# Optimization experiments

Hardware: AMD Instinct MI355X
Metric: run time of the kernel (lower is better)

Reference implementation:

```python
import jax, jax.numpy as jnp
import numpy as np

B, L, HID = 2, 2048, 2048
NH, NKV, HD = 16, 4, 128
LAT = 512
Q_PER_KV = NH // NKV
SCALE = HD ** -0.5
ROPE_THETA = 10000.0


def setup_inputs() -> dict:
    key = jax.random.key(0)
    ks = jax.random.split(key, 6)
    s = lambda fan_in: 1.0 / np.sqrt(fan_in)
    return {
        "x": jax.random.normal(ks[0], (B, L, HID), dtype=jnp.float32),
        "Wq": jax.random.normal(ks[1], (HID, NH * HD), dtype=jnp.float32) * s(HID),
        "Wc": jax.random.normal(ks[2], (HID, LAT), dtype=jnp.float32) * s(HID),
        "Wk": jax.random.normal(ks[3], (LAT, NKV * HD), dtype=jnp.float32) * s(LAT),
        "Wv": jax.random.normal(ks[4], (LAT, NKV * HD), dtype=jnp.float32) * s(LAT),
        "Wo": jax.random.normal(ks[5], (NH * HD, HID), dtype=jnp.float32) * s(NH * HD),
        "attention_mask": jnp.ones((B, L), dtype=jnp.int32),
    }


def _rope(t):  # t: [B, H, L, HD]
    half = HD // 2
    inv_freq = 1.0 / (ROPE_THETA ** (jnp.arange(half, dtype=jnp.float32) / half))
    pos = jnp.arange(t.shape[2], dtype=jnp.float32)
    freqs = pos[:, None] * inv_freq[None, :]          # [L, half]
    cos = jnp.cos(freqs)[None, None].astype(t.dtype)  # [1,1,L,half]
    sin = jnp.sin(freqs)[None, None].astype(t.dtype)
    t1, t2 = t[..., :half], t[..., half:]
    return jnp.concatenate([t1 * cos - t2 * sin, t2 * cos + t1 * sin], axis=-1)


def reference(x, Wq, Wc, Wk, Wv, Wo, attention_mask):
    q = (x @ Wq).reshape(B, L, NH, HD).transpose(0, 2, 1, 3)      # [B,NH,L,HD]
    c = x @ Wc                                                    # latent bottleneck
    k = (c @ Wk).reshape(B, L, NKV, HD).transpose(0, 2, 1, 3)     # [B,NKV,L,HD]
    v = (c @ Wv).reshape(B, L, NKV, HD).transpose(0, 2, 1, 3)
    # GQA repeat_interleave along head axis
    k = jnp.repeat(k, Q_PER_KV, axis=1)                           # [B,NH,L,HD]
    v = jnp.repeat(v, Q_PER_KV, axis=1)
    q = _rope(q)
    k = _rope(k)
    att = jnp.einsum("bhqd,bhkd->bhqk", q, k) * SCALE             # [B,NH,L,L]
    neg = jnp.finfo(att.dtype).min
    causal = jnp.tril(jnp.ones((L, L), dtype=bool))[None, None]
    att = jnp.where(causal, att, neg)
    key_mask = (attention_mask > 0)[:, None, None, :]             # [B,1,1,L]
    att = jnp.where(key_mask, att, neg)
    att = jax.nn.softmax(att, axis=-1)
    y = jnp.einsum("bhqk,bhkd->bhqd", att, v)
    y = y.transpose(0, 2, 1, 3).reshape(B, L, NH * HD)
    return y @ Wo
```

## Files before the change

kernel.cpp:

```cpp
#include <hip/hip_runtime.h>
#include <hip/hip_bf16.h>
#include <cstdint>
#include <cstddef>

#define B_    2
#define L_    2048
#define HID_  2048
#define NH_   16
#define NKV_  4
#define HD_   128
#define LAT_  512
#define SCALE_ 0.08838834764831845f
#define SC2_   0.1275174365f

typedef unsigned short u16;
typedef unsigned int   u32;
typedef __attribute__((ext_vector_type(8))) short   short8;
typedef __attribute__((ext_vector_type(4))) float   floatx4;

typedef __attribute__((address_space(1))) const u32 gas_u32;
typedef __attribute__((address_space(3))) u32       las_u32;

__device__ __forceinline__ void gl_lds16(const u16* g, u16* l) {
    __builtin_amdgcn_global_load_lds((gas_u32*)g, (las_u32*)l, 16, 0, 0);
}

__device__ __forceinline__ float bf2f(u16 u) {
    union { u32 i; float f; } v; v.i = ((u32)u) << 16; return v.f;
}
__device__ __forceinline__ u16 f2bf(float f) {
    union { float f; u32 u; } v; v.f = f;
    u32 u = v.u;
    u32 r = (u + 0x7fffu + ((u >> 16) & 1u)) >> 16;
    return (u16)r;
}

__global__ void cvt_kernel(const float* __restrict__ in, u16* __restrict__ out, int n) {
    int i = blockIdx.x * 256 + threadIdx.x;
    if (i < n) out[i] = f2bf(in[i]);
}

__global__ void cvt_transpose_kernel(const float* __restrict__ in, u16* __restrict__ out,
                                     int R, int C) {
    __shared__ u16 tile[32][33];
    int c0 = blockIdx.x * 32, r0 = blockIdx.y * 32;
    int tx = threadIdx.x & 31, ty = threadIdx.x >> 5;
    for (int i = ty; i < 32; i += 8)
        tile[tx][i] = f2bf(in[(size_t)(r0 + i) * C + c0 + tx]);
    __syncthreads();
    for (int i = ty; i < 32; i += 8)
        out[(size_t)(c0 + i) * R + r0 + tx] = tile[i][tx];
}

__global__ void transpose_v_kernel(const u16* __restrict__ in, u16* __restrict__ out) {
    __shared__ u16 t[32][33];
    int lt = blockIdx.x, dt = blockIdx.y, bh = blockIdx.z;
    int b = bh >> 2, kvh = bh & 3;
    int tx = threadIdx.x & 31, ty = threadIdx.x >> 5;
    for (int i = ty; i < 32; i += 8)
        t[i][tx] = in[(((size_t)b * L_ + lt * 32 + i) * NKV_ + kvh) * HD_ + dt * 32 + tx];
    __syncthreads();
    for (int i = ty; i < 32; i += 8)
        out[((size_t)bh * HD_ + dt * 32 + i) * L_ + lt * 32 + tx] = t[tx][i];
}

template<int OUT_BF16>
__global__ __launch_bounds__(256)
void gemm_bt(const u16* __restrict__ A, const u16* __restrict__ BT,
             void* __restrict__ C, int M, int N, int K) {
    __shared__ __align__(16) u16 As[128][32];
    __shared__ __align__(16) u16 Bs[128][32];
    const int tid  = threadIdx.x;
    const int m0   = blockIdx.y * 128, n0 = blockIdx.x * 128;
    const int wave = tid >> 6, lane = tid & 63;
    const int wm   = (wave >> 1) * 64, wn = (wave & 1) * 64;
    const int quad = lane >> 4, l16 = lane & 15;

    const int srow = wave * 32 + (lane >> 2);
    const int scol = (lane & 3) * 8;
    const u16* aptr0 = A  + (size_t)(m0 + srow) * K + scol;
    const u16* bptr0 = BT + (size_t)(n0 + srow) * K + scol;
    const u16* aptr1 = aptr0 + (size_t)16 * K;
    const u16* bptr1 = bptr0 + (size_t)16 * K;
    u16* lA0 = &As[wave * 32][0];
    u16* lA1 = &As[wave * 32 + 16][0];
    u16* lB0 = &Bs[wave * 32][0];
    u16* lB1 = &Bs[wave * 32 + 16][0];

    floatx4 acc[4][4] = {};

    for (int k0 = 0; k0 < K; k0 += 32) {
        gl_lds16(aptr0 + k0, lA0);
        gl_lds16(aptr1 + k0, lA1);
        gl_lds16(bptr0 + k0, lB0);
        gl_lds16(bptr1 + k0, lB1);
        __syncthreads();

        short8 af[4], bfr[4];
        #pragma unroll
        for (int i = 0; i < 4; i++) af[i]  = *(const short8*)&As[wm + i * 16 + l16][quad * 8];
        #pragma unroll
        for (int i = 0; i < 4; i++) bfr[i] = *(const short8*)&Bs[wn + i * 16 + l16][quad * 8];
        #pragma unroll
        for (int mi = 0; mi < 4; mi++)
            #pragma unroll
            for (int ni = 0; ni < 4; ni++)
                acc[mi][ni] = __builtin_amdgcn_mfma_f32_16x16x32_bf16(
                    af[mi], bfr[ni], acc[mi][ni], 0, 0, 0);
        __syncthreads();
    }

    #pragma unroll
    for (int mi = 0; mi < 4; mi++) {
        #pragma unroll
        for (int ni = 0; ni < 4; ni++) {
            #pragma unroll
            for (int r = 0; r < 4; r++) {
                int row = m0 + wm + mi * 16 + quad * 4 + r;
                int col = n0 + wn + ni * 16 + l16;
                float v = acc[mi][ni][r];
                if (OUT_BF16) ((u16*)C)[(size_t)row * N + col] = f2bf(v);
                else          ((float*)C)[(size_t)row * N + col] = v;
            }
        }
    }
}

__global__ __launch_bounds__(256)
void gemm_bt_split(const u16* __restrict__ A, const u16* __restrict__ BT,
                   u16* __restrict__ C0, u16* __restrict__ C1,
                   int M, int N, int K, int Nsplit, int N0, int N1) {
    __shared__ __align__(16) u16 As[128][32];
    __shared__ __align__(16) u16 Bs[128][32];
    const int tid  = threadIdx.x;
    const int m0   = blockIdx.y * 128, n0 = blockIdx.x * 128;
    const int wave = tid >> 6, lane = tid & 63;
    const int wm   = (wave >> 1) * 64, wn = (wave & 1) * 64;
    const int quad = lane >> 4, l16 = lane & 15;

    const int srow = wave * 32 + (lane >> 2);
    const int scol = (lane & 3) * 8;
    const u16* aptr0 = A  + (size_t)(m0 + srow) * K + scol;
    const u16* bptr0 = BT + (size_t)(n0 + srow) * K + scol;
    const u16* aptr1 = aptr0 + (size_t)16 * K;
    const u16* bptr1 = bptr0 + (size_t)16 * K;
    u16* lA0 = &As[wave * 32][0];
    u16* lA1 = &As[wave * 32 + 16][0];
    u16* lB0 = &Bs[wave * 32][0];
    u16* lB1 = &Bs[wave * 32 + 16][0];

    floatx4 acc[4][4] = {};

    for (int k0 = 0; k0 < K; k0 += 32) {
        gl_lds16(aptr0 + k0, lA0);
        gl_lds16(aptr1 + k0, lA1);
        gl_lds16(bptr0 + k0, lB0);
        gl_lds16(bptr1 + k0, lB1);
        __syncthreads();

        short8 af[4], bfr[4];
        #pragma unroll
        for (int i = 0; i < 4; i++) af[i]  = *(const short8*)&As[wm + i * 16 + l16][quad * 8];
        #pragma unroll
        for (int i = 0; i < 4; i++) bfr[i] = *(const short8*)&Bs[wn + i * 16 + l16][quad * 8];
        #pragma unroll
        for (int mi = 0; mi < 4; mi++)
            #pragma unroll
            for (int ni = 0; ni < 4; ni++)
                acc[mi][ni] = __builtin_amdgcn_mfma_f32_16x16x32_bf16(
                    af[mi], bfr[ni], acc[mi][ni], 0, 0, 0);
        __syncthreads();
    }

    const int side = (n0 >= Nsplit);
    u16* Cw = side ? C1 : C0;
    const int nw = side ? N1 : N0;
    const int cbase = side ? Nsplit : 0;

    #pragma unroll
    for (int mi = 0; mi < 4; mi++) {
        #pragma unroll
        for (int ni = 0; ni < 4; ni++) {
            #pragma unroll
            for (int r = 0; r < 4; r++) {
                int row = m0 + wm + mi * 16 + quad * 4 + r;
                int col = n0 + wn + ni * 16 + l16 - cbase;
                Cw[(size_t)row * nw + col] = f2bf(acc[mi][ni][r]);
            }
        }
    }
}

__global__ void rope_perm(const u16* __restrict__ in, u16* __restrict__ out,
                          int nh, int nhbits) {
    int idx = blockIdx.x * 256 + threadIdx.x;
    int d = idx & 63;
    int l = (idx >> 6) & (L_ - 1);
    int h = (idx >> 17) & (nh - 1);
    int b = idx >> (17 + nhbits);
    const u16* src = &in[(((size_t)b * L_ + l) * nh + h) * HD_];
    u16* dst = &out[(((size_t)b * nh + h) * L_ + l) * HD_];
    float t1 = bf2f(src[d]), t2 = bf2f(src[d + 64]);
    float inv = expf(-(float)d * 0.14391156831212787f);
    float fr = (float)l * inv;
    float c = cosf(fr), sn = sinf(fr);
    dst[d]      = f2bf(t1 * c - t2 * sn);
    dst[d + 64] = f2bf(t2 * c + t1 * sn);
}

__global__ __launch_bounds__(256)
void attn_mfma(const u16* __restrict__ Q, const u16* __restrict__ K,
               const u16* __restrict__ Vt, const int* __restrict__ amask,
               u16* __restrict__ Y, float* __restrict__ Opart,
               float* __restrict__ lpart) {
    __shared__ __align__(16) u16 Ks[64][136];
    __shared__ __align__(16) u16 Vs[128][72];
    __shared__ __align__(16) u16 Ps[4][32][64];
    __shared__ int smask[64];

    const int tid  = threadIdx.x;
    const int wave = tid >> 6, lane = tid & 63;
    const int quad = lane >> 4, l16 = lane & 15;

    const int bid = blockIdx.x;
    const int s   = bid >> 8;
    const int c   = bid & 255;
    const int bkvh = c & 7;
    const int j   = c >> 3;
    const int b   = bkvh >> 2, kvh = bkvh & 3;

    int t, kt0, kt1, pi;
    if (s == 2) {
        t = 31 - j; kt0 = 0; kt1 = (t >> 1) + 1; pi = -1;
    } else {
        t = 32 + j;
        const int nkt = (t >> 1) + 1;
        const int kmid = (nkt + 1) >> 1;
        kt0 = s ? kmid : 0;
        kt1 = s ? nkt  : kmid;
        pi  = c * 2 + s;
    }

    const int h   = kvh * 4 + wave;
    const int q0  = t * 32;

    const u16* Qbase = Q  + ((size_t)b * NH_  + h)   * L_ * HD_;
    const u16* Kbase = K  + ((size_t)b * NKV_ + kvh) * L_ * HD_;
    const u16* Vbase = Vt + ((size_t)b * NKV_ + kvh) * (size_t)HD_ * L_;
    const int* mbase = amask + b * L_;

    short8 qa[2][4];
    #pragma unroll
    for (int mi = 0; mi < 2; ++mi)
        #pragma unroll
        for (int ks = 0; ks < 4; ++ks)
            qa[mi][ks] = *(const short8*)&Qbase[(size_t)(q0 + mi * 16 + l16) * HD_ + ks * 32 + quad * 8];

    floatx4 Oacc[2][8] = {};
    float lsum[2][4] = {};

    const int krow = tid >> 2, kq = (tid & 3) * 32;
    const int vrow = tid >> 1, vh = (tid & 1) * 32;

    const int fr_rd = ((l16 >> 2) & 3) ^ ((l16 & 3) << 1);

    uint4 kr0, kr1, kr2, kr3, vr0, vr1, vr2, vr3;
    int mreg;
    {
        const int kb = kt0 * 64;
        const u16* ksrc = Kbase + (size_t)(kb + krow) * HD_ + kq;
        kr0 = *(const uint4*)(ksrc);
        kr1 = *(const uint4*)(ksrc + 8);
        kr2 = *(const uint4*)(ksrc + 16);
        kr3 = *(const uint4*)(ksrc + 24);
        const u16* vsrc = Vbase + (size_t)vrow * L_ + kb + vh;
        vr0 = *(const uint4*)(vsrc);
        vr1 = *(const uint4*)(vsrc + 8);
        vr2 = *(const uint4*)(vsrc + 16);
        vr3 = *(const uint4*)(vsrc + 24);
        mreg = (tid < 64) ? mbase[kb + tid] : 0;
    }

    for (int kt = kt0; kt < kt1; ++kt) {
        const int kbase = kt * 64;

        *(uint4*)&Ks[krow][kq]      = kr0;
        *(uint4*)&Ks[krow][kq + 8]  = kr1;
        *(uint4*)&Ks[krow][kq + 16] = kr2;
        *(uint4*)&Ks[krow][kq + 24] = kr3;
        *(uint4*)&Vs[vrow][vh]      = vr0;
        *(uint4*)&Vs[vrow][vh + 8]  = vr1;
        *(uint4*)&Vs[vrow][vh + 16] = vr2;
        *(uint4*)&Vs[vrow][vh + 24] = vr3;
        if (tid < 64) smask[tid] = mreg;
        __syncthreads();

        if (kt + 1 < kt1) {
            const int kb = (kt + 1) * 64;
            const u16* ksrc = Kbase + (size_t)(kb + krow) * HD_ + kq;
            kr0 = *(const uint4*)(ksrc);
            kr1 = *(const uint4*)(ksrc + 8);
            kr2 = *(const uint4*)(ksrc + 16);
            kr3 = *(const uint4*)(ksrc + 24);
            const u16* vsrc = Vbase + (size_t)vrow * L_ + kb + vh;
            vr0 = *(const uint4*)(vsrc);
            vr1 = *(const uint4*)(vsrc + 8);
            vr2 = *(const uint4*)(vsrc + 16);
            vr3 = *(const uint4*)(vsrc + 24);
            mreg = (tid < 64) ? mbase[kb + tid] : 0;
        }

        floatx4 sfr[2][4] = {};
        __builtin_amdgcn_s_setprio(1);
        #pragma unroll
        for (int ni = 0; ni < 4; ++ni) {
            #pragma unroll
            for (int ks = 0; ks < 4; ++ks) {
                short8 kf = *(const short8*)&Ks[ni * 16 + l16][ks * 32 + quad * 8];
                sfr[0][ni] = __builtin_amdgcn_mfma_f32_16x16x32_bf16(qa[0][ks], kf, sfr[0][ni], 0, 0, 0);
                sfr[1][ni] = __builtin_amdgcn_mfma_f32_16x16x32_bf16(qa[1][ks], kf, sfr[1][ni], 0, 0, 0);
            }
        }
        __builtin_amdgcn_s_setprio(0);

        int am[4];
        #pragma unroll
        for (int ni = 0; ni < 4; ++ni) am[ni] = smask[ni * 16 + l16];

        #pragma unroll
        for (int mi = 0; mi < 2; ++mi) {
            #pragma unroll
            for (int ni = 0; ni < 4; ++ni) {
                const int kpos = kbase + ni * 16 + l16;
                const bool okm = am[ni] > 0;
                const int blk_log = ni * 2 + (l16 >> 3);
                const int off = l16 & 7;
                #pragma unroll
                for (int r = 0; r < 4; ++r) {
                    const int qrow = q0 + mi * 16 + quad * 4 + r;
                    const bool ok = (kpos <= qrow) & okm;
                    float p = ok ? exp2f(fmaf(sfr[mi][ni][r], SC2_, -8.0f)) : 0.0f;
                    lsum[mi][r] += p;
                    const int pblk = blk_log ^ quad ^ (r << 1);
                    Ps[wave][mi * 16 + quad * 4 + r][pblk * 8 + off] = f2bf(p);
                }
            }
        }

        short8 pf[2][2];
        #pragma unroll
        for (int mi = 0; mi < 2; ++mi)
            #pragma unroll
            for (int kc = 0; kc < 2; ++kc)
                pf[mi][kc] = *(const short8*)&Ps[wave][mi * 16 + l16][(((kc * 4 + quad) ^ fr_rd)) * 8];

        __builtin_amdgcn_s_setprio(1);
        #pragma unroll
        for (int kc = 0; kc < 2; ++kc) {
            #pragma unroll
            for (int dn = 0; dn < 8; ++dn) {
                short8 vf = *(const short8*)&Vs[dn * 16 + l16][kc * 32 + quad * 8];
                Oacc[0][dn] = __builtin_amdgcn_mfma_f32_16x16x32_bf16(pf[0][kc], vf, Oacc[0][dn], 0, 0, 0);
                Oacc[1][dn] = __builtin_amdgcn_mfma_f32_16x16x32_bf16(pf[1][kc], vf, Oacc[1][dn], 0, 0, 0);
            }
        }
        __builtin_amdgcn_s_setprio(0);
        __syncthreads();
    }

    if (pi < 0) {
        #pragma unroll
        for (int mi = 0; mi < 2; ++mi) {
            #pragma unroll
            for (int r = 0; r < 4; ++r) {
                float v = lsum[mi][r];
                v += __shfl_xor(v, 1);
                v += __shfl_xor(v, 2);
                v += __shfl_xor(v, 4);
                v += __shfl_xor(v, 8);
                const float linv = 1.0f / v;
                const int qrow = q0 + mi * 16 + quad * 4 + r;
                u16* dst = &Y[(((size_t)b * L_ + qrow) * NH_ + h) * HD_];
                #pragma unroll
                for (int dn = 0; dn < 8; ++dn)
                    dst[dn * 16 + l16] = f2bf(Oacc[mi][dn][r] * linv);
            }
        }
    } else {
        float* od = Opart + ((size_t)(pi * 4 + wave) * 32) * 128;
        float* lp = lpart + (size_t)(pi * 4 + wave) * 32;
        #pragma unroll
        for (int mi = 0; mi < 2; ++mi) {
            #pragma unroll
            for (int r = 0; r < 4; ++r) {
                float v = lsum[mi][r];
                v += __shfl_xor(v, 1);
                v += __shfl_xor(v, 2);
                v += __shfl_xor(v, 4);
                v += __shfl_xor(v, 8);
                const int qi = mi * 16 + quad * 4 + r;
                if (l16 == 0) lp[qi] = v;
                #pragma unroll
                for (int dn = 0; dn < 8; ++dn)
                    od[(size_t)qi * 128 + dn * 16 + l16] = Oacc[mi][dn][r];
            }
        }
    }
}

__global__ __launch_bounds__(256)
void attn_combine(const float* __restrict__ Opart, const float* __restrict__ lpart,
                  u16* __restrict__ Y) {
    const int cb = blockIdx.x;
    const int c  = cb >> 2, hw = cb & 3;
    const int bkvh = c & 7, j = c >> 3;
    const int b = bkvh >> 2, kvh = bkvh & 3;
    const int h = kvh * 4 + hw;
    const int tid = threadIdx.x;
    const int q = tid >> 3, dg = tid & 7;

    const size_t s0 = ((size_t)(c * 2 + 0) * 4 + hw) * 32 + q;
    const size_t s1 = ((size_t)(c * 2 + 1) * 4 + hw) * 32 + q;
    const float4* o0 = (const float4*)(Opart + s0 * 128 + dg * 16);
    const float4* o1 = (const float4*)(Opart + s1 * 128 + dg * 16);
    const float linv = 1.0f / (lpart[s0] + lpart[s1]);

    const int qrow = (32 + j) * 32 + q;
    u16* dst = &Y[(((size_t)b * L_ + qrow) * NH_ + h) * HD_ + dg * 16];

    u16 tmp[16];
    #pragma unroll
    for (int vv = 0; vv < 4; ++vv) {
        float4 a = o0[vv], bb = o1[vv];
        tmp[vv * 4 + 0] = f2bf((a.x + bb.x) * linv);
        tmp[vv * 4 + 1] = f2bf((a.y + bb.y) * linv);
        tmp[vv * 4 + 2] = f2bf((a.z + bb.z) * linv);
        tmp[vv * 4 + 3] = f2bf((a.w + bb.w) * linv);
    }
    *(uint4*)(dst)     = *(const uint4*)(&tmp[0]);
    *(uint4*)(dst + 8) = *(const uint4*)(&tmp[8]);
}

extern "C" void kernel_launch(void* const* d_in, const int* in_sizes, int n_in,
                              void* d_out, int out_size, void* d_ws, size_t ws_size,
                              hipStream_t stream) {
    const float* x  = (const float*)d_in[0];
    const float* Wq = (const float*)d_in[1];
    const float* Wc = (const float*)d_in[2];
    const float* Wk = (const float*)d_in[3];
    const float* Wv = (const float*)d_in[4];
    const float* Wo = (const float*)d_in[5];
    const int* amask = (const int*)d_in[6];
    float* out = (float*)d_out;

    char* p = (char*)d_ws;
    auto alloc = [&](size_t elems) {
        u16* r = (u16*)p;
        p += ((elems * 2 + 255) / 256) * 256;
        return r;
    };
    u16* Xb   = alloc((size_t)4096 * 2048);
    u16* WqT  = alloc((size_t)2048 * 2048);
    u16* WcT  = alloc((size_t)512 * 2048);
    u16* WkT  = alloc((size_t)512 * 512);
    u16* WvT  = alloc((size_t)512 * 512);
    u16* WoT  = alloc((size_t)2048 * 2048);
    u16* qbuf = alloc((size_t)4096 * 2048);
    u16* Qr   = alloc((size_t)4096 * 2048);
    u16* cbuf = alloc((size_t)4096 * 512);
    u16* kbuf = alloc((size_t)4096 * 512);
    u16* vbuf = alloc((size_t)4096 * 512);
    u16* Kr   = alloc((size_t)4096 * 512);
    u16* Vt   = alloc((size_t)4096 * 512);
    float* Opart = (float*)p; p += (size_t)512 * 4 * 32 * 128 * 4;
    float* lpart = (float*)p; p += (size_t)512 * 4 * 32 * 4;

    cvt_kernel<<<8388608 / 256, 256, 0, stream>>>(x, Xb, 8388608);
    cvt_transpose_kernel<<<dim3(2048 / 32, 2048 / 32), 256, 0, stream>>>(Wq, WqT, 2048, 2048);
    cvt_transpose_kernel<<<dim3(512 / 32, 2048 / 32), 256, 0, stream>>>(Wc, WcT, 2048, 512);
    cvt_transpose_kernel<<<dim3(512 / 32, 512 / 32), 256, 0, stream>>>(Wk, WkT, 512, 512);
    cvt_transpose_kernel<<<dim3(512 / 32, 512 / 32), 256, 0, stream>>>(Wv, WvT, 512, 512);
    cvt_transpose_kernel<<<dim3(2048 / 32, 2048 / 32), 256, 0, stream>>>(Wo, WoT, 2048, 2048);

    gemm_bt_split<<<dim3(20, 32), 256, 0, stream>>>(Xb, WqT, qbuf, cbuf,
                                                    4096, 2560, 2048, 2048, 2048, 512);
    gemm_bt_split<<<dim3(8, 32), 256, 0, stream>>>(cbuf, WkT, kbuf, vbuf,
                                                   4096, 1024, 512, 512, 512, 512);

    rope_perm<<<(2 * 16 * 2048 * 64) / 256, 256, 0, stream>>>(qbuf, Qr, 16, 4);
    rope_perm<<<(2 * 4 * 2048 * 64) / 256, 256, 0, stream>>>(kbuf, Kr, 4, 2);
    transpose_v_kernel<<<dim3(64, 4, 8), 256, 0, stream>>>(vbuf, Vt);

    attn_mfma<<<dim3(768), 256, 0, stream>>>(Qr, Kr, Vt, amask, qbuf, Opart, lpart);
    attn_combine<<<dim3(1024), 256, 0, stream>>>(Opart, lpart, qbuf);

    gemm_bt<0><<<dim3(16, 32), 256, 0, stream>>>(qbuf, WoT, out, 4096, 2048, 2048);
}
```

Baseline: 390.7 us.

## Split attention KV range into five balanced chunks and shrink LDS with swizzle

```diff
diff --git a/kernel.cpp b/kernel.cpp
--- a/kernel.cpp
+++ b/kernel.cpp
@@ -208,14 +208,12 @@
     dst[d + 64] = f2bf(t2 * c + t1 * sn);
 }
 
-__global__ __launch_bounds__(256)
+__global__ __launch_bounds__(256, 4)
 void attn_mfma(const u16* __restrict__ Q, const u16* __restrict__ K,
                const u16* __restrict__ Vt, const int* __restrict__ amask,
-               u16* __restrict__ Y, float* __restrict__ Opart,
-               float* __restrict__ lpart) {
-    __shared__ __align__(16) u16 Ks[64][136];
-    __shared__ __align__(16) u16 Vs[128][72];
-    __shared__ __align__(16) u16 Ps[4][32][64];
+               float* __restrict__ Opart, float* __restrict__ lpart) {
+    __shared__ __align__(16) u16 Ks[64][128];
+    __shared__ __align__(16) u16 Vs[128][64];
     __shared__ int smask[64];
 
     const int tid  = threadIdx.x;
@@ -229,16 +227,14 @@
     const int j   = c >> 3;
     const int b   = bkvh >> 2, kvh = bkvh & 3;
 
-    int t, kt0, kt1, pi;
-    if (s == 2) {
-        t = 31 - j; kt0 = 0; kt1 = (t >> 1) + 1; pi = -1;
-    } else {
-        t = 32 + j;
-        const int nkt = (t >> 1) + 1;
-        const int kmid = (nkt + 1) >> 1;
-        kt0 = s ? kmid : 0;
-        kt1 = s ? nkt  : kmid;
-        pi  = c * 2 + s;
+    const int H  = ((32 + j) >> 1) + 1;
+    const int Lg = ((31 - j) >> 1) + 1;
+    const int nh = (j < 16) ? 3 : 4;
+    int t, kt0, kt1;
+    if (s < nh) { t = 32 + j; kt0 = (H * s) / nh; kt1 = (H * (s + 1)) / nh; }
+    else {
+        const int ls = s - nh, nl = 5 - nh;
+        t = 31 - j; kt0 = (Lg * ls) / nl; kt1 = (Lg * (ls + 1)) / nl;
     }
 
     const int h   = kvh * 4 + wave;
@@ -259,8 +255,11 @@
     floatx4 Oacc[2][8] = {};
     float lsum[2][4] = {};
 
-    const int krow = tid >> 2, kq = (tid & 3) * 32;
-    const int vrow = tid >> 1, vh = (tid & 1) * 32;
+    const int krow = tid >> 2, kq0 = (tid & 3) * 4;
+    const int vrow = tid >> 1, vc0 = (tid & 1) * 4;
+    const int kr7  = krow & 7, vr7 = vrow & 7;
+
+    u16* Psb = &Ks[0][0] + wave * 2048;
 
     const int fr_rd = ((l16 >> 2) & 3) ^ ((l16 & 3) << 1);
 
@@ -268,12 +267,12 @@
     int mreg;
     {
         const int kb = kt0 * 64;
-        const u16* ksrc = Kbase + (size_t)(kb + krow) * HD_ + kq;
+        const u16* ksrc = Kbase + (size_t)(kb + krow) * HD_ + kq0 * 8;
         kr0 = *(const uint4*)(ksrc);
         kr1 = *(const uint4*)(ksrc + 8);
         kr2 = *(const uint4*)(ksrc + 16);
         kr3 = *(const uint4*)(ksrc + 24);
-        const u16* vsrc = Vbase + (size_t)vrow * L_ + kb + vh;
+        const u16* vsrc = Vbase + (size_t)vrow * L_ + kb + vc0 * 8;
         vr0 = *(const uint4*)(vsrc);
         vr1 = *(const uint4*)(vsrc + 8);
         vr2 = *(const uint4*)(vsrc + 16);
@@ -284,25 +283,25 @@
     for (int kt = kt0; kt < kt1; ++kt) {
         const int kbase = kt * 64;
 
-        *(uint4*)&Ks[krow][kq]      = kr0;
-        *(uint4*)&Ks[krow][kq + 8]  = kr1;
-        *(uint4*)&Ks[krow][kq + 16] = kr2;
-        *(uint4*)&Ks[krow][kq + 24] = kr3;
-        *(uint4*)&Vs[vrow][vh]      = vr0;
-        *(uint4*)&Vs[vrow][vh + 8]  = vr1;
-        *(uint4*)&Vs[vrow][vh + 16] = vr2;
-        *(uint4*)&Vs[vrow][vh + 24] = vr3;
+        *(uint4*)&Ks[krow][((kq0 + 0) ^ kr7) * 8] = kr0;
+        *(uint4*)&Ks[krow][((kq0 + 1) ^ kr7) * 8] = kr1;
+        *(uint4*)&Ks[krow][((kq0 + 2) ^ kr7) * 8] = kr2;
+        *(uint4*)&Ks[krow][((kq0 + 3) ^ kr7) * 8] = kr3;
+        *(uint4*)&Vs[vrow][((vc0 + 0) ^ vr7) * 8] = vr0;
+        *(uint4*)&Vs[vrow][((vc0 + 1) ^ vr7) * 8] = vr1;
+        *(uint4*)&Vs[vrow][((vc0 + 2) ^ vr7) * 8] = vr2;
+        *(uint4*)&Vs[vrow][((vc0 + 3) ^ vr7) * 8] = vr3;
         if (tid < 64) smask[tid] = mreg;
         __syncthreads();
 
         if (kt + 1 < kt1) {
             const int kb = (kt + 1) * 64;
-            const u16* ksrc = Kbase + (size_t)(kb + krow) * HD_ + kq;
+            const u16* ksrc = Kbase + (size_t)(kb + krow) * HD_ + kq0 * 8;
             kr0 = *(const uint4*)(ksrc);
             kr1 = *(const uint4*)(ksrc + 8);
             kr2 = *(const uint4*)(ksrc + 16);
             kr3 = *(const uint4*)(ksrc + 24);
-            const u16* vsrc = Vbase + (size_t)vrow * L_ + kb + vh;
+            const u16* vsrc = Vbase + (size_t)vrow * L_ + kb + vc0 * 8;
             vr0 = *(const uint4*)(vsrc);
             vr1 = *(const uint4*)(vsrc + 8);
             vr2 = *(const uint4*)(vsrc + 16);
@@ -316,7 +315,7 @@
         for (int ni = 0; ni < 4; ++ni) {
             #pragma unroll
             for (int ks = 0; ks < 4; ++ks) {
-                short8 kf = *(const short8*)&Ks[ni * 16 + l16][ks * 32 + quad * 8];
+                short8 kf = *(const short8*)&Ks[ni * 16 + l16][((ks * 4 + quad) ^ (l16 & 7)) * 8];
                 sfr[0][ni] = __builtin_amdgcn_mfma_f32_16x16x32_bf16(qa[0][ks], kf, sfr[0][ni], 0, 0, 0);
                 sfr[1][ni] = __builtin_amdgcn_mfma_f32_16x16x32_bf16(qa[1][ks], kf, sfr[1][ni], 0, 0, 0);
             }
@@ -326,6 +325,8 @@
         int am[4];
         #pragma unroll
         for (int ni = 0; ni < 4; ++ni) am[ni] = smask[ni * 16 + l16];
+
+        __syncthreads();
 
         #pragma unroll
         for (int mi = 0; mi < 2; ++mi) {
@@ -342,7 +343,7 @@
                     float p = ok ? exp2f(fmaf(sfr[mi][ni][r], SC2_, -8.0f)) : 0.0f;
                     lsum[mi][r] += p;
                     const int pblk = blk_log ^ quad ^ (r << 1);
-                    Ps[wave][mi * 16 + quad * 4 + r][pblk * 8 + off] = f2bf(p);
+                    Psb[(mi * 16 + quad * 4 + r) * 64 + pblk * 8 + off] = f2bf(p);
                 }
             }
         }
@@ -352,14 +353,14 @@
         for (int mi = 0; mi < 2; ++mi)
             #pragma unroll
             for (int kc = 0; kc < 2; ++kc)
-                pf[mi][kc] = *(const short8*)&Ps[wave][mi * 16 + l16][(((kc * 4 + quad) ^ fr_rd)) * 8];
+                pf[mi][kc] = *(const short8*)&Psb[(mi * 16 + l16) * 64 + ((kc * 4 + quad) ^ fr_rd) * 8];
 
         __builtin_amdgcn_s_setprio(1);
         #pragma unroll
         for (int kc = 0; kc < 2; ++kc) {
             #pragma unroll
             for (int dn = 0; dn < 8; ++dn) {
-                short8 vf = *(const short8*)&Vs[dn * 16 + l16][kc * 32 + quad * 8];
+                short8 vf = *(const short8*)&Vs[dn * 16 + l16][((kc * 4 + quad) ^ (l16 & 7)) * 8];
                 Oacc[0][dn] = __builtin_amdgcn_mfma_f32_16x16x32_bf16(pf[0][kc], vf, Oacc[0][dn], 0, 0, 0);
                 Oacc[1][dn] = __builtin_amdgcn_mfma_f32_16x16x32_bf16(pf[1][kc], vf, Oacc[1][dn], 0, 0, 0);
             }
@@ -368,42 +369,22 @@
         __syncthreads();
     }
 
-    if (pi < 0) {
-        #pragma unroll
-        for (int mi = 0; mi < 2; ++mi) {
-            #pragma unroll
-            for (int r = 0; r < 4; ++r) {
-                float v = lsum[mi][r];
-                v += __shfl_xor(v, 1);
-                v += __shfl_xor(v, 2);
-                v += __shfl_xor(v, 4);
-                v += __shfl_xor(v, 8);
-                const float linv = 1.0f / v;
-                const int qrow = q0 + mi * 16 + quad * 4 + r;
-                u16* dst = &Y[(((size_t)b * L_ + qrow) * NH_ + h) * HD_];
-                #pragma unroll
-                for (int dn = 0; dn < 8; ++dn)
-                    dst[dn * 16 + l16] = f2bf(Oacc[mi][dn][r] * linv);
-            }
-        }
-    } else {
-        float* od = Opart + ((size_t)(pi * 4 + wave) * 32) * 128;
-        float* lp = lpart + (size_t)(pi * 4 + wave) * 32;
-        #pragma unroll
-        for (int mi = 0; mi < 2; ++mi) {
-            #pragma unroll
-            for (int r = 0; r < 4; ++r) {
-                float v = lsum[mi][r];
-                v += __shfl_xor(v, 1);
-                v += __shfl_xor(v, 2);
-                v += __shfl_xor(v, 4);
-                v += __shfl_xor(v, 8);
-                const int qi = mi * 16 + quad * 4 + r;
-                if (l16 == 0) lp[qi] = v;
-                #pragma unroll
-                for (int dn = 0; dn < 8; ++dn)
-                    od[(size_t)qi * 128 + dn * 16 + l16] = Oacc[mi][dn][r];
-            }
+    float* od = Opart + ((size_t)bid * 4 + wave) * 32 * 128;
+    float* lp = lpart + ((size_t)bid * 4 + wave) * 32;
+    #pragma unroll
+    for (int mi = 0; mi < 2; ++mi) {
+        #pragma unroll
+        for (int r = 0; r < 4; ++r) {
+            float v = lsum[mi][r];
+            v += __shfl_xor(v, 1);
+            v += __shfl_xor(v, 2);
+            v += __shfl_xor(v, 4);
+            v += __shfl_xor(v, 8);
+            const int qi = mi * 16 + quad * 4 + r;
+            if (l16 == 0) lp[qi] = v;
+            #pragma unroll
+            for (int dn = 0; dn < 8; ++dn)
+                od[(size_t)qi * 128 + dn * 16 + l16] = Oacc[mi][dn][r];
         }
     }
 }
@@ -412,31 +393,43 @@
 void attn_combine(const float* __restrict__ Opart, const float* __restrict__ lpart,
                   u16* __restrict__ Y) {
     const int cb = blockIdx.x;
-    const int c  = cb >> 2, hw = cb & 3;
+    const int c  = cb & 255, z = cb >> 8;
+    const int tile = z >> 2, hw = z & 3;
     const int bkvh = c & 7, j = c >> 3;
     const int b = bkvh >> 2, kvh = bkvh & 3;
     const int h = kvh * 4 + hw;
+    const int nh = (j < 16) ? 3 : 4;
+    const int s0 = tile ? nh : 0;
+    const int ns = tile ? (5 - nh) : nh;
+    const int t  = tile ? (31 - j) : (32 + j);
     const int tid = threadIdx.x;
     const int q = tid >> 3, dg = tid & 7;
 
-    const size_t s0 = ((size_t)(c * 2 + 0) * 4 + hw) * 32 + q;
-    const size_t s1 = ((size_t)(c * 2 + 1) * 4 + hw) * 32 + q;
-    const float4* o0 = (const float4*)(Opart + s0 * 128 + dg * 16);
-    const float4* o1 = (const float4*)(Opart + s1 * 128 + dg * 16);
-    const float linv = 1.0f / (lpart[s0] + lpart[s1]);
-
-    const int qrow = (32 + j) * 32 + q;
+    float4 a0 = {0,0,0,0}, a1 = {0,0,0,0}, a2 = {0,0,0,0}, a3 = {0,0,0,0};
+    float lacc = 0.0f;
+    for (int i = 0; i < ns; ++i) {
+        const size_t rowb = ((size_t)((s0 + i) * 256 + c) * 4 + hw) * 32 + q;
+        lacc += lpart[rowb];
+        const float4* op = (const float4*)(Opart + rowb * 128 + dg * 16);
+        float4 v0 = op[0], v1 = op[1], v2 = op[2], v3 = op[3];
+        a0.x += v0.x; a0.y += v0.y; a0.z += v0.z; a0.w += v0.w;
+        a1.x += v1.x; a1.y += v1.y; a1.z += v1.z; a1.w += v1.w;
+        a2.x += v2.x; a2.y += v2.y; a2.z += v2.z; a2.w += v2.w;
+        a3.x += v3.x; a3.y += v3.y; a3.z += v3.z; a3.w += v3.w;
+    }
+    const float linv = 1.0f / lacc;
+    const int qrow = t * 32 + q;
     u16* dst = &Y[(((size_t)b * L_ + qrow) * NH_ + h) * HD_ + dg * 16];
 
     u16 tmp[16];
-    #pragma unroll
-    for (int vv = 0; vv < 4; ++vv) {
-        float4 a = o0[vv], bb = o1[vv];
-        tmp[vv * 4 + 0] = f2bf((a.x + bb.x) * linv);
-        tmp[vv * 4 + 1] = f2bf((a.y + bb.y) * linv);
-        tmp[vv * 4 + 2] = f2bf((a.z + bb.z) * linv);
-        tmp[vv * 4 + 3] = f2bf((a.w + bb.w) * linv);
-    }
+    tmp[0]  = f2bf(a0.x * linv); tmp[1]  = f2bf(a0.y * linv);
+    tmp[2]  = f2bf(a0.z * linv); tmp[3]  = f2bf(a0.w * linv);
+    tmp[4]  = f2bf(a1.x * linv); tmp[5]  = f2bf(a1.y * linv);
+    tmp[6]  = f2bf(a1.z * linv); tmp[7]  = f2bf(a1.w * linv);
+    tmp[8]  = f2bf(a2.x * linv); tmp[9]  = f2bf(a2.y * linv);
+    tmp[10] = f2bf(a2.z * linv); tmp[11] = f2bf(a2.w * linv);
+    tmp[12] = f2bf(a3.x * linv); tmp[13] = f2bf(a3.y * linv);
+    tmp[14] = f2bf(a3.z * linv); tmp[15] = f2bf(a3.w * linv);
     *(uint4*)(dst)     = *(const uint4*)(&tmp[0]);
     *(uint4*)(dst + 8) = *(const uint4*)(&tmp[8]);
 }
@@ -459,21 +452,22 @@
         p += ((elems * 2 + 255) / 256) * 256;
         return r;
     };
+    u16* WoT  = alloc((size_t)2048 * 2048);
+    u16* qbuf = alloc((size_t)4096 * 2048);
+    u16* Qr   = alloc((size_t)4096 * 2048);
+    u16* Kr   = alloc((size_t)4096 * 512);
+    u16* Vt   = alloc((size_t)4096 * 512);
+    char* pdead = p;
     u16* Xb   = alloc((size_t)4096 * 2048);
     u16* WqT  = alloc((size_t)2048 * 2048);
     u16* WcT  = alloc((size_t)512 * 2048);
     u16* WkT  = alloc((size_t)512 * 512);
     u16* WvT  = alloc((size_t)512 * 512);
-    u16* WoT  = alloc((size_t)2048 * 2048);
-    u16* qbuf = alloc((size_t)4096 * 2048);
-    u16* Qr   = alloc((size_t)4096 * 2048);
     u16* cbuf = alloc((size_t)4096 * 512);
     u16* kbuf = alloc((size_t)4096 * 512);
     u16* vbuf = alloc((size_t)4096 * 512);
-    u16* Kr   = alloc((size_t)4096 * 512);
-    u16* Vt   = alloc((size_t)4096 * 512);
-    float* Opart = (float*)p; p += (size_t)512 * 4 * 32 * 128 * 4;
-    float* lpart = (float*)p; p += (size_t)512 * 4 * 32 * 4;
+    float* Opart = (float*)pdead;
+    float* lpart = (float*)(pdead + (size_t)1280 * 4 * 32 * 128 * 4);
 
     cvt_kernel<<<8388608 / 256, 256, 0, stream>>>(x, Xb, 8388608);
     cvt_transpose_kernel<<<dim3(2048 / 32, 2048 / 32), 256, 0, stream>>>(Wq, WqT, 2048, 2048);
@@ -491,8 +485,8 @@
     rope_perm<<<(2 * 4 * 2048 * 64) / 256, 256, 0, stream>>>(kbuf, Kr, 4, 2);
     transpose_v_kernel<<<dim3(64, 4, 8), 256, 0, stream>>>(vbuf, Vt);
 
-    attn_mfma<<<dim3(768), 256, 0, stream>>>(Qr, Kr, Vt, amask, qbuf, Opart, lpart);
-    attn_combine<<<dim3(1024), 256, 0, stream>>>(Opart, lpart, qbuf);
+    attn_mfma<<<dim3(1280), 256, 0, stream>>>(Qr, Kr, Vt, amask, Opart, lpart);
+    attn_combine<<<dim3(2048), 256, 0, stream>>>(Opart, lpart, qbuf);
 
     gemm_bt<0><<<dim3(16, 32), 256, 0, stream>>>(qbuf, WoT, out, 4096, 2048, 2048);
 }
```

After: 607.3 us. 1.55x slower.
